# Kernel optimization log

Hardware: AMD Instinct MI355X
Metric: run time of the kernel (lower is better)

The kernel has to match this reference:

```python
import jax, jax.numpy as jnp
import numpy as np

B, T, D, H = 131072, 16, 2, 64  # batch, horizon, event dim, GRU hidden


def setup_inputs() -> dict:
    key = jax.random.key(0)
    ks = jax.random.split(key, 10)
    s = 1.0 / np.sqrt(H)
    u = lambda k, shape: jax.random.uniform(k, shape, jnp.float32, -s, s)
    return {
        "x": jax.random.normal(ks[0], (B, T, D), jnp.float32),   # base-dist samples
        "z": jax.random.normal(ks[1], (B, H), jnp.float32),      # context / GRU state
        # nn.GRUCell(input_size=D, hidden_size=H) params (torch layout)
        "W_ih": u(ks[2], (3 * H, D)),
        "W_hh": u(ks[3], (3 * H, H)),
        "b_ih": u(ks[4], (3 * H,)),
        "b_hh": u(ks[5], (3 * H,)),
        # locscale MLP: H -> 32 -> 4
        "W1": u(ks[6], (H, 32)),
        "b1": u(ks[7], (32,)),
        "W2": u(ks[8], (32, 4)),
        "b2": u(ks[9], (4,)),
    }


def reference(x, z, W_ih, W_hh, b_ih, b_hh, W1, b1, W2, b2):
    """AutoregressiveFlow._forward: base samples x -> data samples y, logabsdet."""
    Bb, Tt, Dd = x.shape

    def gru(inp, h):  # PyTorch GRUCell semantics
        gi = inp @ W_ih.T + b_ih          # [B, 3H]
        gh = h @ W_hh.T + b_hh            # [B, 3H]
        i_r, i_z, i_n = jnp.split(gi, 3, axis=-1)
        h_r, h_z, h_n = jnp.split(gh, 3, axis=-1)
        r = jax.nn.sigmoid(i_r + h_r)
        u = jax.nn.sigmoid(i_z + h_z)
        n = jnp.tanh(i_n + r * h_n)
        return (1.0 - u) * n + u * h

    def step(carry, x_t):
        h, y_tm1 = carry
        h = gru(y_tm1, h)
        hid = jax.nn.relu(h @ W1 + b1)            # [B, 32]
        ls = hid @ W2 + b2                        # [B, 4]
        dloc = ls[:, :2]
        scale = jax.nn.softplus(ls[:, 2:]) + 0.001
        y_t = y_tm1 + dloc + scale * x_t
        return (h, y_t), (y_t, scale)

    init = (z, jnp.zeros((Bb, Dd), x.dtype))
    _, (y, scales) = jax.lax.scan(step, init, jnp.swapaxes(x, 0, 1))
    y = jnp.swapaxes(y, 0, 1)          # [B, T, D]
    scales = jnp.swapaxes(scales, 0, 1)
    logabsdet = jnp.sum(jnp.log(jnp.abs(jnp.prod(scales, axis=-2))), axis=-1)  # [B]
    return y, logabsdet
```

## Files before the change

### kernel.cpp

```cpp
#include <hip/hip_runtime.h>

#define BSZ 131072
#define TT  16
#define RPB 64
#define BLK 256

typedef __bf16 bf16x8 __attribute__((ext_vector_type(8)));
typedef float  f32x4  __attribute__((ext_vector_type(4)));

#define MFMA(a, b, c) __builtin_amdgcn_mfma_f32_16x16x32_bf16((a), (b), (c), 0, 0, 0)

__device__ __forceinline__ float rcp_fast(float xx) {
    float r; asm("v_rcp_f32 %0, %1" : "=v"(r) : "v"(xx)); return r;
}
__device__ __forceinline__ float sigmoid_f(float v) { return rcp_fast(1.0f + __expf(-v)); }
__device__ __forceinline__ float tanh_f(float v)    { return 1.0f - 2.0f * rcp_fast(1.0f + __expf(2.0f * v)); }

__global__ __launch_bounds__(BLK, 2) void flow_mfma(
    const float* __restrict__ x,
    const float* __restrict__ z,
    const float* __restrict__ W_ih,
    const float* __restrict__ W_hh,
    const float* __restrict__ b_ih,
    const float* __restrict__ b_hh,
    const float* __restrict__ W1,
    const float* __restrict__ b1,
    const float* __restrict__ W2,
    const float* __restrict__ b2,
    float* __restrict__ y_out,
    float* __restrict__ lad_out)
{
    __shared__ __align__(16) __bf16 hbuf[RPB * 72];
    __shared__ __align__(16) __bf16 hidbuf[RPB * 40];
    __shared__ __align__(16) float4 gi_tab[192];
    __shared__ __align__(16) float  lsbuf[RPB * 4];
    __shared__ __align__(16) float2 ystate[RPB];
    __shared__ __align__(16) float2 ybuf[RPB * TT];

    const int tid  = threadIdx.x;
    const int lane = tid & 63, wave = tid >> 6;
    const int quad = lane >> 4, n16 = lane & 15;
    const int gb   = blockIdx.x * RPB;
    const f32x4 zero = {0.f, 0.f, 0.f, 0.f};

    if (tid < 192) {
        const int j = tid;
        const float w0 = W_ih[2*j], w1 = W_ih[2*j+1];
        const float bi = b_ih[j], bh = b_hh[j];
        gi_tab[j] = (j < 128) ? make_float4(w0, w1, bi + bh, 0.f)
                              : make_float4(w0, w1, bi, bh);
    }
    if (tid < RPB) ystate[tid] = make_float2(0.f, 0.f);

    #pragma unroll
    for (int r4 = 0; r4 < 4; ++r4) {
        const int row = (tid >> 4) + r4 * 16;
        const int col = (tid & 15) * 4;
        const float4 zv = *(const float4*)&z[(size_t)(gb + row) * 64 + col];
        hbuf[row*72 + col + 0] = (__bf16)zv.x;
        hbuf[row*72 + col + 1] = (__bf16)zv.y;
        hbuf[row*72 + col + 2] = (__bf16)zv.z;
        hbuf[row*72 + col + 3] = (__bf16)zv.w;
    }

    bf16x8 Whh[12][2];
    #pragma unroll
    for (int ct = 0; ct < 12; ++ct)
        #pragma unroll
        for (int kt = 0; kt < 2; ++kt) {
            const float* p = W_hh + (size_t)(ct*16 + n16) * 64 + kt*32 + quad*8;
            bf16x8 f;
            #pragma unroll
            for (int j = 0; j < 8; ++j) f[j] = (__bf16)p[j];
            Whh[ct][kt] = f;
        }
    bf16x8 W1f[2][2];
    #pragma unroll
    for (int c2 = 0; c2 < 2; ++c2)
        #pragma unroll
        for (int kt = 0; kt < 2; ++kt) {
            bf16x8 f;
            #pragma unroll
            for (int j = 0; j < 8; ++j)
                f[j] = (__bf16)W1[(size_t)(kt*32 + quad*8 + j) * 32 + c2*16 + n16];
            W1f[c2][kt] = f;
        }
    bf16x8 W2f;
    #pragma unroll
    for (int j = 0; j < 8; ++j)
        W2f[j] = (n16 < 4) ? (__bf16)W2[(size_t)(quad*8 + j) * 4 + n16] : (__bf16)0.f;

    const float b1v0 = b1[n16], b1v1 = b1[16 + n16];
    const float4 b2v = *(const float4*)b2;

    f32x4 hst[4];
    #pragma unroll
    for (int ct = 0; ct < 4; ++ct)
        #pragma unroll
        for (int i = 0; i < 4; ++i)
            hst[ct][i] = z[(size_t)(gb + wave*16 + quad*4 + i) * 64 + ct*16 + n16];

    __syncthreads();

    float y0 = 0.f, y1 = 0.f, lad = 0.f;
    const float* xrow = x + (size_t)(gb + wave*16 + lane) * (TT*2);
    const int arow = wave*16 + n16;

    #pragma unroll 1
    for (int t = 0; t < TT; ++t) {
        bf16x8 a0 = *(const bf16x8*)&hbuf[arow*72 + quad*8];
        bf16x8 a1 = *(const bf16x8*)&hbuf[arow*72 + 32 + quad*8];

        float ys0[4], ys1[4];
        #pragma unroll
        for (int i = 0; i < 4; ++i) {
            const float2 yv = ystate[wave*16 + quad*4 + i];
            ys0[i] = yv.x; ys1[i] = yv.y;
        }

        #pragma unroll
        for (int g = 0; g < 4; ++g) {
            f32x4 cr = MFMA(a0, Whh[g  ][0], zero); cr = MFMA(a1, Whh[g  ][1], cr);
            f32x4 cz = MFMA(a0, Whh[g+4][0], zero); cz = MFMA(a1, Whh[g+4][1], cz);
            f32x4 cn = MFMA(a0, Whh[g+8][0], zero); cn = MFMA(a1, Whh[g+8][1], cn);
            const float4 Tr = gi_tab[      g*16 + n16];
            const float4 Tz = gi_tab[ 64 + g*16 + n16];
            const float4 Tn = gi_tab[128 + g*16 + n16];
            #pragma unroll
            for (int i = 0; i < 4; ++i) {
                const float gir = fmaf(Tr.x, ys0[i], fmaf(Tr.y, ys1[i], Tr.z));
                const float giz = fmaf(Tz.x, ys0[i], fmaf(Tz.y, ys1[i], Tz.z));
                const float gin = fmaf(Tn.x, ys0[i], fmaf(Tn.y, ys1[i], Tn.z));
                const float r  = sigmoid_f(gir + cr[i]);
                const float u  = sigmoid_f(giz + cz[i]);
                const float nn = tanh_f(fmaf(r, cn[i] + Tn.w, gin));
                const float hv = fmaf(u, hst[g][i] - nn, nn);
                hst[g][i] = hv;
                hbuf[(wave*16 + quad*4 + i)*72 + g*16 + n16] = (__bf16)hv;
            }
        }

        bf16x8 h0 = *(const bf16x8*)&hbuf[arow*72 + quad*8];
        bf16x8 h1 = *(const bf16x8*)&hbuf[arow*72 + 32 + quad*8];
        #pragma unroll
        for (int c2 = 0; c2 < 2; ++c2) {
            f32x4 hc = MFMA(h0, W1f[c2][0], zero); hc = MFMA(h1, W1f[c2][1], hc);
            const float bb = c2 ? b1v1 : b1v0;
            #pragma unroll
            for (int i = 0; i < 4; ++i) {
                const float v = fmaxf(hc[i] + bb, 0.f);
                hidbuf[(wave*16 + quad*4 + i)*40 + c2*16 + n16] = (__bf16)v;
            }
        }

        bf16x8 ha = *(const bf16x8*)&hidbuf[arow*40 + quad*8];
        f32x4 ls = MFMA(ha, W2f, zero);
        if (n16 < 4) {
            #pragma unroll
            for (int i = 0; i < 4; ++i)
                lsbuf[(wave*16 + quad*4 + i)*4 + n16] = ls[i];
        }

        if (lane < 16) {
            const int rl = wave*16 + lane;
            const float4 L = *(const float4*)&lsbuf[rl*4];
            const float l0 = L.x + b2v.x, l1 = L.y + b2v.y;
            const float l2 = L.z + b2v.z, l3 = L.w + b2v.w;
            const float s0 = __logf(1.0f + __expf(l2)) + 0.001f;
            const float s1 = __logf(1.0f + __expf(l3)) + 0.001f;
            const float2 xt = *(const float2*)&xrow[t*2];
            y0 += l0 + s0 * xt.x;
            y1 += l1 + s1 * xt.y;
            lad += __logf(s0) + __logf(s1);
            ystate[rl] = make_float2(y0, y1);
            ybuf[rl*TT + t] = make_float2(y0, y1);
        }
    }

    const float4* yb4 = (const float4*)ybuf;
    float4* yg4 = (float4*)(y_out + (size_t)gb * (TT*2));
    #pragma unroll
    for (int it = 0; it < 2; ++it) {
        const int idx = wave*128 + it*64 + lane;
        yg4[idx] = yb4[idx];
    }
    if (lane < 16) lad_out[gb + wave*16 + lane] = lad;
}

extern "C" void kernel_launch(void* const* d_in, const int* in_sizes, int n_in,
                              void* d_out, int out_size, void* d_ws, size_t ws_size,
                              hipStream_t stream) {
    const float* x    = (const float*)d_in[0];
    const float* z    = (const float*)d_in[1];
    const float* W_ih = (const float*)d_in[2];
    const float* W_hh = (const float*)d_in[3];
    const float* b_ih = (const float*)d_in[4];
    const float* b_hh = (const float*)d_in[5];
    const float* W1   = (const float*)d_in[6];
    const float* b1   = (const float*)d_in[7];
    const float* W2   = (const float*)d_in[8];
    const float* b2   = (const float*)d_in[9];

    float* y_out   = (float*)d_out;
    float* lad_out = y_out + (size_t)BSZ * TT * 2;

    dim3 grid(BSZ / RPB), block(BLK);
    hipLaunchKernelGGL(flow_mfma, grid, block, 0, stream,
                       x, z, W_ih, W_hh, b_ih, b_hh, W1, b1, W2, b2,
                       y_out, lad_out);
}
```

Measured before the change: 289.5 us.

## Raise occupancy: move W1/W2 fragments to LDS, fold biases into MFMA accumulators

Launch bounds go from 2 to 3 blocks per SM to raise occupancy. To free registers, the W1 and W2 MFMA fragments now live in shared-memory tables instead of VGPRs, and the b_hh n-gate, b1 and b2 biases seed the MFMA accumulators, which removes separate adds. The epilogue now spreads the two output components across 32 lanes instead of 16 and reuses the h fragments read from LDS across timesteps. In exchange, each timestep issues extra LDS reads for the weights, and register pressure under the tighter bound could cause spills.

Result: slower. 532.8 us (+84.0%).

```diff
diff --git a/kernel.cpp b/kernel.cpp
--- a/kernel.cpp
+++ b/kernel.cpp
@@ -8,15 +8,13 @@
 typedef __bf16 bf16x8 __attribute__((ext_vector_type(8)));
 typedef float  f32x4  __attribute__((ext_vector_type(4)));
 
-#define MFMA(a, b, c) __builtin_amdgcn_mfma_f32_16x16x32_bf16((a), (b), (c), 0, 0, 0)
-
-__device__ __forceinline__ float rcp_fast(float xx) {
-    float r; asm("v_rcp_f32 %0, %1" : "=v"(r) : "v"(xx)); return r;
-}
-__device__ __forceinline__ float sigmoid_f(float v) { return rcp_fast(1.0f + __expf(-v)); }
-__device__ __forceinline__ float tanh_f(float v)    { return 1.0f - 2.0f * rcp_fast(1.0f + __expf(2.0f * v)); }
-
-__global__ __launch_bounds__(BLK, 2) void flow_mfma(
+#define MFMA(a,b,c) __builtin_amdgcn_mfma_f32_16x16x32_bf16((a),(b),(c),0,0,0)
+
+static __device__ __forceinline__ float rcp_f(float v){ float r; asm("v_rcp_f32 %0, %1" : "=v"(r) : "v"(v)); return r; }
+static __device__ __forceinline__ float sigm(float v){ return rcp_f(1.0f + __expf(-v)); }
+static __device__ __forceinline__ float tanh_f(float v){ return 1.0f - 2.0f*rcp_f(1.0f + __expf(2.0f*v)); }
+
+__global__ __launch_bounds__(BLK, 3) void flow3(
     const float* __restrict__ x,
     const float* __restrict__ z,
     const float* __restrict__ W_ih,
@@ -30,182 +28,187 @@
     float* __restrict__ y_out,
     float* __restrict__ lad_out)
 {
-    __shared__ __align__(16) __bf16 hbuf[RPB * 72];
-    __shared__ __align__(16) __bf16 hidbuf[RPB * 40];
-    __shared__ __align__(16) float4 gi_tab[192];
-    __shared__ __align__(16) float  lsbuf[RPB * 4];
-    __shared__ __align__(16) float2 ystate[RPB];
-    __shared__ __align__(16) float2 ybuf[RPB * TT];
-
-    const int tid  = threadIdx.x;
-    const int lane = tid & 63, wave = tid >> 6;
-    const int quad = lane >> 4, n16 = lane & 15;
-    const int gb   = blockIdx.x * RPB;
-    const f32x4 zero = {0.f, 0.f, 0.f, 0.f};
-
-    if (tid < 192) {
-        const int j = tid;
-        const float w0 = W_ih[2*j], w1 = W_ih[2*j+1];
-        const float bi = b_ih[j], bh = b_hh[j];
-        gi_tab[j] = (j < 128) ? make_float4(w0, w1, bi + bh, 0.f)
-                              : make_float4(w0, w1, bi, bh);
-    }
-    if (tid < RPB) ystate[tid] = make_float2(0.f, 0.f);
-
-    #pragma unroll
-    for (int r4 = 0; r4 < 4; ++r4) {
-        const int row = (tid >> 4) + r4 * 16;
-        const int col = (tid & 15) * 4;
-        const float4 zv = *(const float4*)&z[(size_t)(gb + row) * 64 + col];
-        hbuf[row*72 + col + 0] = (__bf16)zv.x;
-        hbuf[row*72 + col + 1] = (__bf16)zv.y;
-        hbuf[row*72 + col + 2] = (__bf16)zv.z;
-        hbuf[row*72 + col + 3] = (__bf16)zv.w;
-    }
-
-    bf16x8 Whh[12][2];
-    #pragma unroll
-    for (int ct = 0; ct < 12; ++ct)
-        #pragma unroll
-        for (int kt = 0; kt < 2; ++kt) {
-            const float* p = W_hh + (size_t)(ct*16 + n16) * 64 + kt*32 + quad*8;
-            bf16x8 f;
-            #pragma unroll
-            for (int j = 0; j < 8; ++j) f[j] = (__bf16)p[j];
-            Whh[ct][kt] = f;
-        }
-    bf16x8 W1f[2][2];
-    #pragma unroll
-    for (int c2 = 0; c2 < 2; ++c2)
-        #pragma unroll
-        for (int kt = 0; kt < 2; ++kt) {
-            bf16x8 f;
-            #pragma unroll
-            for (int j = 0; j < 8; ++j)
-                f[j] = (__bf16)W1[(size_t)(kt*32 + quad*8 + j) * 32 + c2*16 + n16];
-            W1f[c2][kt] = f;
-        }
-    bf16x8 W2f;
+  __shared__ __align__(16) __bf16 hbuf[RPB*72];
+  __shared__ __align__(16) __bf16 hidbuf[RPB*40];
+  __shared__ __align__(16) float4 gi_tab[192];
+  __shared__ __align__(16) __bf16 w1tab[4*64*8];
+  __shared__ __align__(16) __bf16 w2tab[64*8];
+  __shared__ __align__(16) float  lsbuf[RPB*4];
+  __shared__ __align__(16) float  ystate[RPB*2];
+  __shared__ __align__(16) float  ybuf[RPB*34];
+
+  const int tid  = threadIdx.x;
+  const int lane = tid & 63, wave = tid >> 6;
+  const int quad = lane >> 4, n16 = lane & 15;
+  const int gb   = blockIdx.x * RPB;
+  const f32x4 zero = {0.f,0.f,0.f,0.f};
+
+  if (tid < 192) {
+    const int j = tid;
+    const float w0 = W_ih[2*j], w1 = W_ih[2*j+1];
+    const float bi = b_ih[j], bh = b_hh[j];
+    gi_tab[j] = make_float4(w0, w1, (j < 128) ? bi + bh : bi, 0.f);
+  }
+  {
+    const int f = tid >> 6, c2 = f >> 1, kt = f & 1;
+    bf16x8 v;
     #pragma unroll
     for (int j = 0; j < 8; ++j)
-        W2f[j] = (n16 < 4) ? (__bf16)W2[(size_t)(quad*8 + j) * 4 + n16] : (__bf16)0.f;
-
-    const float b1v0 = b1[n16], b1v1 = b1[16 + n16];
-    const float4 b2v = *(const float4*)b2;
-
-    f32x4 hst[4];
-    #pragma unroll
-    for (int ct = 0; ct < 4; ++ct)
+      v[j] = (__bf16)W1[(size_t)(kt*32 + quad*8 + j)*32 + c2*16 + n16];
+    *(bf16x8*)&w1tab[(f*64 + lane)*8] = v;
+  }
+  if (tid < 64) {
+    bf16x8 v;
+    #pragma unroll
+    for (int j = 0; j < 8; ++j)
+      v[j] = (n16 < 4) ? (__bf16)W2[(size_t)(quad*8 + j)*4 + n16] : (__bf16)0.f;
+    *(bf16x8*)&w2tab[lane*8] = v;
+  }
+  if (tid < 128) ystate[tid] = 0.f;
+  #pragma unroll
+  for (int r4 = 0; r4 < 4; ++r4) {
+    const int row = (tid >> 4) + r4*16, col = (tid & 15)*4;
+    const float4 zv = *(const float4*)&z[(size_t)(gb + row)*64 + col];
+    hbuf[row*72 + col+0] = (__bf16)zv.x; hbuf[row*72 + col+1] = (__bf16)zv.y;
+    hbuf[row*72 + col+2] = (__bf16)zv.z; hbuf[row*72 + col+3] = (__bf16)zv.w;
+  }
+
+  bf16x8 Whh[12][2];
+  #pragma unroll
+  for (int ct = 0; ct < 12; ++ct)
+    #pragma unroll
+    for (int kt = 0; kt < 2; ++kt) {
+      const float* p = W_hh + (size_t)(ct*16 + n16)*64 + kt*32 + quad*8;
+      bf16x8 f;
+      #pragma unroll
+      for (int j = 0; j < 8; ++j) f[j] = (__bf16)p[j];
+      Whh[ct][kt] = f;
+    }
+  f32x4 hst[4];
+  #pragma unroll
+  for (int g = 0; g < 4; ++g)
+    #pragma unroll
+    for (int i = 0; i < 4; ++i)
+      hst[g][i] = z[(size_t)(gb + wave*16 + quad*4 + i)*64 + g*16 + n16];
+  float bhn[4];
+  #pragma unroll
+  for (int g = 0; g < 4; ++g) bhn[g] = b_hh[128 + g*16 + n16];
+  const float b1v0 = b1[n16], b1v1 = b1[16 + n16];
+  const float b2ln = (n16 < 4) ? b2[n16] : 0.f;
+
+  __syncthreads();
+
+  const int arow = wave*16 + n16;
+  bf16x8 a0 = *(const bf16x8*)&hbuf[arow*72 + quad*8];
+  bf16x8 a1 = *(const bf16x8*)&hbuf[arow*72 + 32 + quad*8];
+
+  const int erow = wave*16 + (lane & 15);
+  const int comp = (lane >> 4) & 1;
+  const float* xp = x + (size_t)(gb + erow)*(TT*2) + comp;
+  float yc = 0.f, lad = 0.f;
+
+  #pragma unroll 1
+  for (int t = 0; t < TT; ++t) {
+    float ys0[4], ys1[4];
+    #pragma unroll
+    for (int i = 0; i < 4; ++i) {
+      ys0[i] = ystate[(wave*16 + quad*4 + i)*2];
+      ys1[i] = ystate[(wave*16 + quad*4 + i)*2 + 1];
+    }
+
+    #pragma unroll
+    for (int g = 0; g < 4; ++g) {
+      f32x4 cr = MFMA(a0, Whh[g  ][0], zero); cr = MFMA(a1, Whh[g  ][1], cr);
+      f32x4 cz = MFMA(a0, Whh[g+4][0], zero); cz = MFMA(a1, Whh[g+4][1], cz);
+      const f32x4 cninit = {bhn[g], bhn[g], bhn[g], bhn[g]};
+      f32x4 cn = MFMA(a0, Whh[g+8][0], cninit); cn = MFMA(a1, Whh[g+8][1], cn);
+      const float4 Tr = gi_tab[      g*16 + n16];
+      const float4 Tz = gi_tab[ 64 + g*16 + n16];
+      const float4 Tn = gi_tab[128 + g*16 + n16];
+      #pragma unroll
+      for (int i = 0; i < 4; ++i) {
+        const float gir = fmaf(Tr.x, ys0[i], fmaf(Tr.y, ys1[i], Tr.z));
+        const float giz = fmaf(Tz.x, ys0[i], fmaf(Tz.y, ys1[i], Tz.z));
+        const float gin = fmaf(Tn.x, ys0[i], fmaf(Tn.y, ys1[i], Tn.z));
+        const float r  = sigm(gir + cr[i]);
+        const float u  = sigm(giz + cz[i]);
+        const float nn = tanh_f(fmaf(r, cn[i], gin));
+        const float hv = fmaf(u, hst[g][i] - nn, nn);
+        hst[g][i] = hv;
+        hbuf[(wave*16 + quad*4 + i)*72 + g*16 + n16] = (__bf16)hv;
+      }
+    }
+
+    a0 = *(const bf16x8*)&hbuf[arow*72 + quad*8];
+    a1 = *(const bf16x8*)&hbuf[arow*72 + 32 + quad*8];
+
+    #pragma unroll
+    for (int c2 = 0; c2 < 2; ++c2) {
+      const float bb = c2 ? b1v1 : b1v0;
+      const f32x4 binit = {bb, bb, bb, bb};
+      f32x4 hc = MFMA(a0, *(const bf16x8*)&w1tab[((c2*2  )*64 + lane)*8], binit);
+      hc       = MFMA(a1, *(const bf16x8*)&w1tab[((c2*2+1)*64 + lane)*8], hc);
+      #pragma unroll
+      for (int i = 0; i < 4; ++i)
+        hidbuf[(wave*16 + quad*4 + i)*40 + c2*16 + n16] = (__bf16)fmaxf(hc[i], 0.f);
+    }
+
+    {
+      const bf16x8 ha = *(const bf16x8*)&hidbuf[arow*40 + quad*8];
+      const f32x4 b2init = {b2ln, b2ln, b2ln, b2ln};
+      const f32x4 ls = MFMA(ha, *(const bf16x8*)&w2tab[lane*8], b2init);
+      if (n16 < 4) {
         #pragma unroll
         for (int i = 0; i < 4; ++i)
-            hst[ct][i] = z[(size_t)(gb + wave*16 + quad*4 + i) * 64 + ct*16 + n16];
-
-    __syncthreads();
-
-    float y0 = 0.f, y1 = 0.f, lad = 0.f;
-    const float* xrow = x + (size_t)(gb + wave*16 + lane) * (TT*2);
-    const int arow = wave*16 + n16;
-
-    #pragma unroll 1
-    for (int t = 0; t < TT; ++t) {
-        bf16x8 a0 = *(const bf16x8*)&hbuf[arow*72 + quad*8];
-        bf16x8 a1 = *(const bf16x8*)&hbuf[arow*72 + 32 + quad*8];
-
-        float ys0[4], ys1[4];
-        #pragma unroll
-        for (int i = 0; i < 4; ++i) {
-            const float2 yv = ystate[wave*16 + quad*4 + i];
-            ys0[i] = yv.x; ys1[i] = yv.y;
-        }
-
-        #pragma unroll
-        for (int g = 0; g < 4; ++g) {
-            f32x4 cr = MFMA(a0, Whh[g  ][0], zero); cr = MFMA(a1, Whh[g  ][1], cr);
-            f32x4 cz = MFMA(a0, Whh[g+4][0], zero); cz = MFMA(a1, Whh[g+4][1], cz);
-            f32x4 cn = MFMA(a0, Whh[g+8][0], zero); cn = MFMA(a1, Whh[g+8][1], cn);
-            const float4 Tr = gi_tab[      g*16 + n16];
-            const float4 Tz = gi_tab[ 64 + g*16 + n16];
-            const float4 Tn = gi_tab[128 + g*16 + n16];
-            #pragma unroll
-            for (int i = 0; i < 4; ++i) {
-                const float gir = fmaf(Tr.x, ys0[i], fmaf(Tr.y, ys1[i], Tr.z));
-                const float giz = fmaf(Tz.x, ys0[i], fmaf(Tz.y, ys1[i], Tz.z));
-                const float gin = fmaf(Tn.x, ys0[i], fmaf(Tn.y, ys1[i], Tn.z));
-                const float r  = sigmoid_f(gir + cr[i]);
-                const float u  = sigmoid_f(giz + cz[i]);
-                const float nn = tanh_f(fmaf(r, cn[i] + Tn.w, gin));
-                const float hv = fmaf(u, hst[g][i] - nn, nn);
-                hst[g][i] = hv;
-                hbuf[(wave*16 + quad*4 + i)*72 + g*16 + n16] = (__bf16)hv;
-            }
-        }
-
-        bf16x8 h0 = *(const bf16x8*)&hbuf[arow*72 + quad*8];
-        bf16x8 h1 = *(const bf16x8*)&hbuf[arow*72 + 32 + quad*8];
-        #pragma unroll
-        for (int c2 = 0; c2 < 2; ++c2) {
-            f32x4 hc = MFMA(h0, W1f[c2][0], zero); hc = MFMA(h1, W1f[c2][1], hc);
-            const float bb = c2 ? b1v1 : b1v0;
-            #pragma unroll
-            for (int i = 0; i < 4; ++i) {
-                const float v = fmaxf(hc[i] + bb, 0.f);
-                hidbuf[(wave*16 + quad*4 + i)*40 + c2*16 + n16] = (__bf16)v;
-            }
-        }
-
-        bf16x8 ha = *(const bf16x8*)&hidbuf[arow*40 + quad*8];
-        f32x4 ls = MFMA(ha, W2f, zero);
-        if (n16 < 4) {
-            #pragma unroll
-            for (int i = 0; i < 4; ++i)
-                lsbuf[(wave*16 + quad*4 + i)*4 + n16] = ls[i];
-        }
-
-        if (lane < 16) {
-            const int rl = wave*16 + lane;
-            const float4 L = *(const float4*)&lsbuf[rl*4];
-            const float l0 = L.x + b2v.x, l1 = L.y + b2v.y;
-            const float l2 = L.z + b2v.z, l3 = L.w + b2v.w;
-            const float s0 = __logf(1.0f + __expf(l2)) + 0.001f;
-            const float s1 = __logf(1.0f + __expf(l3)) + 0.001f;
-            const float2 xt = *(const float2*)&xrow[t*2];
-            y0 += l0 + s0 * xt.x;
-            y1 += l1 + s1 * xt.y;
-            lad += __logf(s0) + __logf(s1);
-            ystate[rl] = make_float2(y0, y1);
-            ybuf[rl*TT + t] = make_float2(y0, y1);
-        }
-    }
-
-    const float4* yb4 = (const float4*)ybuf;
-    float4* yg4 = (float4*)(y_out + (size_t)gb * (TT*2));
-    #pragma unroll
-    for (int it = 0; it < 2; ++it) {
-        const int idx = wave*128 + it*64 + lane;
-        yg4[idx] = yb4[idx];
-    }
-    if (lane < 16) lad_out[gb + wave*16 + lane] = lad;
+          lsbuf[(wave*16 + quad*4 + i)*4 + n16] = ls[i];
+      }
+    }
+
+    if (lane < 32) {
+      const float lc = lsbuf[erow*4 + comp];
+      const float l2 = lsbuf[erow*4 + 2 + comp];
+      const float s  = __logf(1.0f + __expf(l2)) + 0.001f;
+      const float xt = xp[t*2];
+      yc += lc + s * xt;
+      lad += __logf(s);
+      ystate[erow*2 + comp] = yc;
+      ybuf[erow*34 + t*2 + comp] = yc;
+    }
+  }
+
+  const float lado = __shfl(lad, lane ^ 16, 64);
+  if (lane < 16) lad_out[gb + wave*16 + lane] = lad + lado;
+
+  #pragma unroll
+  for (int it = 0; it < 4; ++it) {
+    const int n = it*64 + lane;
+    const int row = n >> 4, tt = n & 15;
+    float2 v;
+    v.x = ybuf[(wave*16 + row)*34 + tt*2];
+    v.y = ybuf[(wave*16 + row)*34 + tt*2 + 1];
+    *(float2*)&y_out[(size_t)(gb + wave*16 + row)*32 + tt*2] = v;
+  }
 }
 
 extern "C" void kernel_launch(void* const* d_in, const int* in_sizes, int n_in,
                               void* d_out, int out_size, void* d_ws, size_t ws_size,
                               hipStream_t stream) {
-    const float* x    = (const float*)d_in[0];
-    const float* z    = (const float*)d_in[1];
-    const float* W_ih = (const float*)d_in[2];
-    const float* W_hh = (const float*)d_in[3];
-    const float* b_ih = (const float*)d_in[4];
-    const float* b_hh = (const float*)d_in[5];
-    const float* W1   = (const float*)d_in[6];
-    const float* b1   = (const float*)d_in[7];
-    const float* W2   = (const float*)d_in[8];
-    const float* b2   = (const float*)d_in[9];
-
-    float* y_out   = (float*)d_out;
-    float* lad_out = y_out + (size_t)BSZ * TT * 2;
-
-    dim3 grid(BSZ / RPB), block(BLK);
-    hipLaunchKernelGGL(flow_mfma, grid, block, 0, stream,
-                       x, z, W_ih, W_hh, b_ih, b_hh, W1, b1, W2, b2,
-                       y_out, lad_out);
+  const float* x    = (const float*)d_in[0];
+  const float* z    = (const float*)d_in[1];
+  const float* W_ih = (const float*)d_in[2];
+  const float* W_hh = (const float*)d_in[3];
+  const float* b_ih = (const float*)d_in[4];
+  const float* b_hh = (const float*)d_in[5];
+  const float* W1   = (const float*)d_in[6];
+  const float* b1   = (const float*)d_in[7];
+  const float* W2   = (const float*)d_in[8];
+  const float* b2   = (const float*)d_in[9];
+
+  float* y_out   = (float*)d_out;
+  float* lad_out = y_out + (size_t)BSZ * TT * 2;
+
+  dim3 grid(BSZ / RPB), block(BLK);
+  hipLaunchKernelGGL(flow3, grid, block, 0, stream,
+                     x, z, W_ih, W_hh, b_ih, b_hh, W1, b1, W2, b2,
+                     y_out, lad_out);
 }
```
